# Optimization experiments

Hardware: AMD Instinct MI355X
Metric: run time of the kernel (lower is better)

Reference implementation:

```python
import jax, jax.numpy as jnp
import numpy as np

B, S, D, H = 4, 2048, 512, 8
HD = D // H
POOL_HEADS = 8


def setup_inputs() -> dict:
    key = jax.random.key(0)
    ks = iter(jax.random.split(key, 32))
    p = {}
    p['x'] = jax.random.normal(next(ks), (B, S, D), dtype=jnp.float32)
    p['mask'] = jnp.zeros((B, S), dtype=jnp.float32)  # key_padding_mask (1.0 = padded)
    s = 1.0 / np.sqrt(D)
    for layer in ('1', '2'):
        for name in ('q', 'k', 'v', 'o'):
            p[f'{name}{layer}_w'] = jax.random.normal(next(ks), (D, D), dtype=jnp.float32) * s
            p[f'{name}{layer}_b'] = jnp.zeros((D,), dtype=jnp.float32)
    p['ln1_g'] = jnp.ones((D,), jnp.float32); p['ln1_b'] = jnp.zeros((D,), jnp.float32)
    p['ffn_w1'] = jax.random.normal(next(ks), (D, D), dtype=jnp.float32) * s
    p['ffn_b1'] = jnp.zeros((D,), jnp.float32)
    p['ffn_w2'] = jax.random.normal(next(ks), (D, D), dtype=jnp.float32) * s
    p['ffn_b2'] = jnp.zeros((D,), jnp.float32)
    p['ln2_g'] = jnp.ones((D,), jnp.float32); p['ln2_b'] = jnp.zeros((D,), jnp.float32)
    p['pool_w'] = jax.random.normal(next(ks), (D, POOL_HEADS), dtype=jnp.float32) * s
    p['pool_b'] = jnp.zeros((POOL_HEADS,), jnp.float32)
    return p


def _layernorm(x, g, b, eps=1e-5):
    mu = jnp.mean(x, axis=-1, keepdims=True)
    var = jnp.var(x, axis=-1, keepdims=True)
    return (x - mu) * jax.lax.rsqrt(var + eps) * g + b


def _mha(x, mask, qw, qb, kw, kb, vw, vb, ow, ob):
    b, s, d = x.shape
    q = (x @ qw + qb).reshape(b, s, H, HD)
    k = (x @ kw + kb).reshape(b, s, H, HD)
    v = (x @ vw + vb).reshape(b, s, H, HD)
    scores = jnp.einsum('bihd,bjhd->bhij', q, k) / jnp.sqrt(jnp.float32(HD))
    scores = scores - mask[:, None, None, :] * 1e30  # key_padding_mask
    w = jax.nn.softmax(scores, axis=-1)  # dropout is identity at eval
    out = jnp.einsum('bhij,bjhd->bihd', w, v).reshape(b, s, d)
    return out @ ow + ob


def _pool(x, mask, pw, pb):
    alpha = jax.nn.leaky_relu(x @ pw + pb)            # [B,S,POOL_HEADS]
    alpha = alpha + mask[:, :, None] * -1e16
    alpha = jax.nn.softmax(alpha, axis=1)             # softmax over sequence
    # sum over heads of alpha_h * x, then sum over sequence
    return jnp.einsum('bs,bsd->bd', alpha.sum(axis=-1), x)


def reference(x, mask,
              q1_w, q1_b, k1_w, k1_b, v1_w, v1_b, o1_w, o1_b,
              q2_w, q2_b, k2_w, k2_b, v2_w, v2_b, o2_w, o2_b,
              ln1_g, ln1_b, ffn_w1, ffn_b1, ffn_w2, ffn_b2,
              ln2_g, ln2_b, pool_w, pool_b):
    # F.normalize(x, p=2, dim=-1)
    x = x / jnp.maximum(jnp.linalg.norm(x, axis=-1, keepdims=True), 1e-12)
    h = _mha(x, mask, q1_w, q1_b, k1_w, k1_b, v1_w, v1_b, o1_w, o1_b)
    h = _layernorm(h, ln1_g, ln1_b)
    h = jax.nn.relu(h @ ffn_w1 + ffn_b1) @ ffn_w2 + ffn_b2
    h = _mha(h, mask, q2_w, q2_b, k2_w, k2_b, v2_w, v2_b, o2_w, o2_b)
    h = _layernorm(h, ln2_g, ln2_b)
    return _pool(h, mask, pool_w, pool_b)  # [B, D] patch_feature (cls=False -> logit is None)
```

## Files before the change

kernel.cpp:

```cpp
#include <hip/hip_runtime.h>
#include <hip/hip_bf16.h>
#include <stdint.h>

#define DEVI __device__ __forceinline__

typedef float f32x4 __attribute__((ext_vector_type(4)));
typedef float f32x16 __attribute__((ext_vector_type(16)));
typedef short bf16x8 __attribute__((ext_vector_type(8)));

typedef __attribute__((address_space(3))) unsigned int as3_u32;
typedef __attribute__((address_space(1))) unsigned int as1_u32;

DEVI void gload16(const void* g, void* l) {
  __builtin_amdgcn_global_load_lds((const as1_u32*)g, (as3_u32*)l, 16, 0, 0);
}

DEVI unsigned short bf16r(float f) {
  union { float f; unsigned int u; } v; v.f = f;
  unsigned int u = v.u;
  return (unsigned short)((u + 0x7FFFu + ((u >> 16) & 1u)) >> 16);
}

DEVI unsigned int pkbf16(float a, float b) {
  __hip_bfloat162 h = __float22bfloat162_rn(make_float2(a, b));
  return *(unsigned int*)&h;
}

struct PrepArgs {
  const float* w[10];
  const float* b1[3];
  const float* b2[3];
};

__global__ __launch_bounds__(256) void prep_kernel(PrepArgs pa, unsigned short* wt,
                                                   float* qb1, float* qb2) {
  __shared__ float lt[64][65];
  const int slot = blockIdx.z;
  const int n0 = blockIdx.x * 64, k0 = blockIdx.y * 64;
  const float* W = pa.w[slot];
  for (int it = 0; it < 16; it++) {
    int idx = it * 256 + threadIdx.x;
    int kr = idx >> 6, nc = idx & 63;
    lt[kr][nc] = W[(long)(k0 + kr) * 512 + n0 + nc];
  }
  __syncthreads();
  unsigned short* dst = wt + (long)slot * 512 * 512;
  for (int it = 0; it < 16; it++) {
    int idx = it * 256 + threadIdx.x;
    int nr = idx >> 6, kc = idx & 63;
    dst[(long)(n0 + nr) * 512 + k0 + kc] = bf16r(lt[kc][nr]);
  }
  if (blockIdx.x == 0 && blockIdx.y == 0) {
    if (slot < 3) {
      for (int i = threadIdx.x; i < 512; i += 256) qb1[slot * 512 + i] = pa.b1[slot][i];
    } else if (slot >= 6 && slot < 9) {
      for (int i = threadIdx.x; i < 512; i += 256) qb2[(slot - 6) * 512 + i] = pa.b2[slot - 6][i];
    }
  }
}

__global__ __launch_bounds__(256) void l2norm_kernel(const float* __restrict__ x,
                                                     unsigned short* __restrict__ xn) {
  const long row = blockIdx.x;
  const float* xr = x + row * 512;
  float v0 = xr[threadIdx.x], v1 = xr[threadIdx.x + 256];
  float ss = v0 * v0 + v1 * v1;
  #pragma unroll
  for (int off = 32; off > 0; off >>= 1) ss += __shfl_down(ss, off, 64);
  __shared__ float red[4];
  __shared__ float sc[1];
  int w = threadIdx.x >> 6, ln = threadIdx.x & 63;
  if (ln == 0) red[w] = ss;
  __syncthreads();
  if (threadIdx.x == 0) {
    float S = red[0] + red[1] + red[2] + red[3];
    sc[0] = 1.0f / fmaxf(sqrtf(S), 1e-12f);
  }
  __syncthreads();
  float s = sc[0];
  xn[row * 512 + threadIdx.x] = bf16r(v0 * s);
  xn[row * 512 + threadIdx.x + 256] = bf16r(v1 * s);
}

template <int EPI>
__global__ __launch_bounds__(256) void gemm_bt(const unsigned short* __restrict__ A,
                                               const unsigned short* __restrict__ Bt,
                                               const float* __restrict__ bias,
                                               void* __restrict__ Cv, int K, int N,
                                               unsigned short* __restrict__ vtout) {
  __shared__ unsigned short ldsA[128 * 64];
  __shared__ unsigned short ldsB[128 * 64];
  const int tid = threadIdx.x, w = tid >> 6, ln = tid & 63;
  const int bm = blockIdx.x, bn = blockIdx.y;
  const int wm = (w >> 1) * 64, wn = (w & 1) * 64;
  const f32x4 zf = {0.f, 0.f, 0.f, 0.f};
  f32x4 acc[4][4];
  #pragma unroll
  for (int i = 0; i < 4; i++)
    #pragma unroll
    for (int j = 0; j < 4; j++) acc[i][j] = zf;
  const int r8 = ln >> 3, s8 = ln & 7;
  for (int kt = 0; kt < K; kt += 64) {
    #pragma unroll
    for (int i = 0; i < 4; i++) {
      int row = w * 32 + i * 8 + r8;
      gload16(A + (long)(bm * 128 + row) * K + kt + s8 * 8, &ldsA[(w * 32 + i * 8) * 64]);
      gload16(Bt + (long)(bn * 128 + row) * K + kt + s8 * 8, &ldsB[(w * 32 + i * 8) * 64]);
    }
    __syncthreads();
    #pragma unroll
    for (int kk = 0; kk < 2; kk++) {
      bf16x8 af[4], bfr[4];
      #pragma unroll
      for (int mf = 0; mf < 4; mf++) {
        int row = wm + mf * 16 + (ln & 15);
        af[mf] = *(const bf16x8*)&ldsA[row * 64 + kk * 32 + (ln >> 4) * 8];
      }
      #pragma unroll
      for (int nf = 0; nf < 4; nf++) {
        int row = wn + nf * 16 + (ln & 15);
        bfr[nf] = *(const bf16x8*)&ldsB[row * 64 + kk * 32 + (ln >> 4) * 8];
      }
      #pragma unroll
      for (int mf = 0; mf < 4; mf++)
        #pragma unroll
        for (int nf = 0; nf < 4; nf++)
          acc[mf][nf] = __builtin_amdgcn_mfma_f32_16x16x32_bf16(af[mf], bfr[nf], acc[mf][nf], 0, 0, 0);
    }
    __syncthreads();
  }
  const int g = ln >> 4, c = ln & 15;
  #pragma unroll
  for (int mf = 0; mf < 4; mf++) {
    #pragma unroll
    for (int nf = 0; nf < 4; nf++) {
      int col = bn * 128 + wn + nf * 16 + c;
      float bv = bias[col];
      if (EPI == 3 && col >= 1024) {
        long row0 = bm * 128 + wm + mf * 16 + g * 4;
        int b = (int)(row0 >> 11), s = (int)(row0 & 2047);
        int vc = col - 1024, h = vc >> 6, hd = vc & 63;
        ushort4 o;
        o.x = bf16r(acc[mf][nf][0] + bv);
        o.y = bf16r(acc[mf][nf][1] + bv);
        o.z = bf16r(acc[mf][nf][2] + bv);
        o.w = bf16r(acc[mf][nf][3] + bv);
        *(ushort4*)(vtout + ((long)((b * 8 + h) * 64 + hd)) * 2048 + s) = o;
      } else {
        #pragma unroll
        for (int j = 0; j < 4; j++) {
          long row = bm * 128 + wm + mf * 16 + g * 4 + j;
          float v = acc[mf][nf][j] + bv;
          if (EPI == 2) v = v > 0.f ? v : 0.f;
          if (EPI == 0)
            ((float*)Cv)[row * N + col] = v;
          else
            ((unsigned short*)Cv)[row * N + col] = bf16r(v);
        }
      }
    }
  }
}

template <int EPI>
__global__ __launch_bounds__(256) void gemm_bt64(const unsigned short* __restrict__ A,
                                                 const unsigned short* __restrict__ Bt,
                                                 const float* __restrict__ bias,
                                                 void* __restrict__ Cv, int K, int N) {
  __shared__ unsigned short ldsA[128 * 64];
  __shared__ unsigned short ldsB[64 * 64];
  const int tid = threadIdx.x, w = tid >> 6, ln = tid & 63;
  const int bm = blockIdx.x, bn = blockIdx.y;
  const int wm = (w >> 1) * 64, wn = (w & 1) * 32;
  const f32x4 zf = {0.f, 0.f, 0.f, 0.f};
  f32x4 acc[4][2];
  #pragma unroll
  for (int i = 0; i < 4; i++)
    #pragma unroll
    for (int j = 0; j < 2; j++) acc[i][j] = zf;
  const int r8 = ln >> 3, s8 = ln & 7;
  for (int kt = 0; kt < K; kt += 64) {
    #pragma unroll
    for (int i = 0; i < 6; i++) {
      int jj = w * 6 + i;
      if (jj < 16) {
        gload16(A + (long)(bm * 128 + jj * 8 + r8) * K + kt + s8 * 8, &ldsA[jj * 512]);
      } else {
        int jb = jj - 16;
        gload16(Bt + (long)(bn * 64 + jb * 8 + r8) * K + kt + s8 * 8, &ldsB[jb * 512]);
      }
    }
    __syncthreads();
    #pragma unroll
    for (int kk = 0; kk < 2; kk++) {
      bf16x8 af[4], bfr[2];
      #pragma unroll
      for (int mf = 0; mf < 4; mf++)
        af[mf] = *(const bf16x8*)&ldsA[(wm + mf * 16 + (ln & 15)) * 64 + kk * 32 + (ln >> 4) * 8];
      #pragma unroll
      for (int nf = 0; nf < 2; nf++)
        bfr[nf] = *(const bf16x8*)&ldsB[(wn + nf * 16 + (ln & 15)) * 64 + kk * 32 + (ln >> 4) * 8];
      #pragma unroll
      for (int mf = 0; mf < 4; mf++)
        #pragma unroll
        for (int nf = 0; nf < 2; nf++)
          acc[mf][nf] = __builtin_amdgcn_mfma_f32_16x16x32_bf16(af[mf], bfr[nf], acc[mf][nf], 0, 0, 0);
    }
    __syncthreads();
  }
  const int g = ln >> 4, c = ln & 15;
  #pragma unroll
  for (int mf = 0; mf < 4; mf++) {
    #pragma unroll
    for (int nf = 0; nf < 2; nf++) {
      int col = bn * 64 + wn + nf * 16 + c;
      float bv = bias[col];
      #pragma unroll
      for (int j = 0; j < 4; j++) {
        long row = bm * 128 + wm + mf * 16 + g * 4 + j;
        float v = acc[mf][nf][j] + bv;
        if (EPI == 2) v = v > 0.f ? v : 0.f;
        if (EPI == 0)
          ((float*)Cv)[row * N + col] = v;
        else
          ((unsigned short*)Cv)[row * N + col] = bf16r(v);
      }
    }
  }
}

__global__ __launch_bounds__(256, 4) void attn_kernel(
    const unsigned short* __restrict__ qkv,
    const unsigned short* __restrict__ vt,
    const float* __restrict__ mask,
    unsigned short* __restrict__ ao) {
  const int tid = threadIdx.x, w = tid >> 6, ln = tid & 63;
  const int lo = ln & 31, hi = ln >> 5;
  const int bid = blockIdx.x + 16 * blockIdx.y;
  const int swz = (bid & 7) * 64 + (bid >> 3);
  const int qb = swz & 15, bh = swz >> 4;
  const int b = bh >> 3, h = bh & 7;
  const int q0 = qb * 128 + w * 32;
  const unsigned short* qp = qkv + (long)(b * 2048) * 1536 + h * 64;
  const unsigned short* kp = qp + 512;
  const unsigned short* vtp = vt + (long)bh * 64 * 2048;
  const float* mp = mask + b * 2048;

  __shared__ unsigned short sbuf[2][4096];
  __shared__ float mbuf[2048];
  __shared__ int mflag;

  {
    float acc = 0.f;
    #pragma unroll
    for (int i = 0; i < 8; i++) {
      float mv = mp[i * 256 + tid];
      mbuf[i * 256 + tid] = mv;
      acc += fabsf(mv);
    }
    if (tid == 0) mflag = 0;
    __syncthreads();
    if (acc != 0.f) mflag = 1;
    __syncthreads();
  }
  const bool anymask = (mflag != 0);

  const int jj0 = w * 2;
  const char *src0, *src1;
  long step;
  if (w < 2) {
    int r0 = jj0 * 8 + (ln >> 3), r1 = r0 + 8, s = ln & 7;
    src0 = (const char*)kp + 2L * ((long)r0 * 1536 + ((s ^ (r0 & 7)) * 8));
    src1 = (const char*)kp + 2L * ((long)r1 * 1536 + ((s ^ (r1 & 7)) * 8));
    step = 32L * 1536 * 2;
  } else {
    int j0 = (w - 2) * 2;
    int r0 = j0 * 16 + (ln >> 2), r1 = r0 + 16, s = ln & 3;
    src0 = (const char*)vtp + 2L * ((long)r0 * 2048 + ((s ^ ((r0 >> 1) & 3)) * 8));
    src1 = (const char*)vtp + 2L * ((long)r1 * 2048 + ((s ^ ((r1 >> 1) & 3)) * 8));
    step = 64;
  }
  unsigned short* const d0a = &sbuf[0][jj0 * 512];
  unsigned short* const d0b = d0a + 512;
  unsigned short* const d1a = &sbuf[1][jj0 * 512];
  unsigned short* const d1b = d1a + 512;

  int koffe[4];
  #pragma unroll
  for (int t = 0; t < 4; t++)
    koffe[t] = lo * 64 + (((t * 2 + hi) ^ (lo & 7)) * 8);
  int voffe[4];
  #pragma unroll
  for (int stt = 0; stt < 2; stt++)
    #pragma unroll
    for (int tau = 0; tau < 2; tau++) {
      int vr = tau * 32 + lo;
      voffe[stt * 2 + tau] = 2048 + vr * 32 + ((((stt * 2 + hi) ^ ((vr >> 1) & 3))) * 8);
    }

  bf16x8 qf[4];
  #pragma unroll
  for (int t = 0; t < 4; t++)
    qf[t] = *(const bf16x8*)(qp + (long)(q0 + lo) * 1536 + t * 16 + hi * 8);

  f32x16 oacc[2];
  #pragma unroll
  for (int t = 0; t < 2; t++)
    #pragma unroll
    for (int r = 0; r < 16; r++) oacc[t][r] = 0.f;
  float lsum = 0.f;
  const f32x16 zf16 = oacc[0];
  const float SC = 0.18033688011112042f;

  gload16(src0, d0a);
  gload16(src1, d0b);
  src0 += step; src1 += step;

#define ATTN_BODY(CURB, DA, DB, ITOFF, STAGE_NEXT)                              \
  {                                                                             \
    if (STAGE_NEXT) {                                                           \
      gload16(src0, DA);                                                        \
      gload16(src1, DB);                                                        \
      src0 += step; src1 += step;                                               \
      asm volatile("s_waitcnt vmcnt(2)" ::: "memory");                          \
    } else {                                                                    \
      asm volatile("s_waitcnt vmcnt(0)" ::: "memory");                          \
    }                                                                           \
    __builtin_amdgcn_s_barrier();                                               \
    __builtin_amdgcn_sched_barrier(0);                                          \
    f32x16 sacc = zf16;                                                         \
    _Pragma("unroll")                                                           \
    for (int t = 0; t < 4; t++) {                                               \
      bf16x8 kf = *(const bf16x8*)&sbuf[CURB][koffe[t]];                        \
      sacc = __builtin_amdgcn_mfma_f32_32x32x16_bf16(kf, qf[t], sacc, 0, 0, 0); \
    }                                                                           \
    float e[16];                                                                \
    _Pragma("unroll")                                                           \
    for (int r = 0; r < 16; r++) e[r] = sacc[r] * SC;                           \
    if (anymask) {                                                              \
      float mval = mbuf[(ITOFF) + lo];                                          \
      _Pragma("unroll")                                                         \
      for (int r = 0; r < 16; r++)                                              \
        e[r] -= 1.4426950408889634e30f *                                        \
                __shfl(mval, (r & 3) + 8 * (r >> 2) + 4 * hi, 64);              \
    }                                                                           \
    _Pragma("unroll")                                                           \
    for (int r = 0; r < 16; r++) e[r] = __builtin_amdgcn_exp2f(e[r]);           \
    _Pragma("unroll")                                                           \
    for (int r = 0; r < 16; r++) lsum += e[r];                                  \
    unsigned int cv[8];                                                         \
    _Pragma("unroll")                                                           \
    for (int i = 0; i < 8; i++) cv[i] = pkbf16(e[2 * i], e[2 * i + 1]);         \
    _Pragma("unroll")                                                           \
    for (int stt = 0; stt < 2; stt++) {                                         \
      unsigned int pf[4];                                                       \
      {                                                                         \
        auto r0_ = __builtin_amdgcn_permlane32_swap(cv[stt * 4 + 0],            \
                                                    cv[stt * 4 + 2], false, false); \
        auto r1_ = __builtin_amdgcn_permlane32_swap(cv[stt * 4 + 1],            \
                                                    cv[stt * 4 + 3], false, false); \
        pf[0] = r0_[0]; pf[1] = r1_[0]; pf[2] = r0_[1]; pf[3] = r1_[1];         \
      }                                                                         \
      bf16x8 pfr = *(const bf16x8*)pf;                                          \
      _Pragma("unroll")                                                         \
      for (int tau = 0; tau < 2; tau++) {                                       \
        bf16x8 vf = *(const bf16x8*)&sbuf[CURB][voffe[stt * 2 + tau]];          \
        oacc[tau] = __builtin_amdgcn_mfma_f32_32x32x16_bf16(vf, pfr, oacc[tau], 0, 0, 0); \
      }                                                                         \
    }                                                                           \
    __builtin_amdgcn_sched_barrier(0);                                          \
    __builtin_amdgcn_s_barrier();                                               \
  }

  for (int it2 = 0; it2 < 32; it2++) {
    ATTN_BODY(0, d1a, d1b, it2 * 64, 1)
    ATTN_BODY(1, d0a, d0b, it2 * 64 + 32, (it2 < 31))
  }
#undef ATTN_BODY

  lsum += __shfl_xor(lsum, 32, 64);
  const float inv = 1.f / lsum;
  unsigned short* ob = ao + ((long)(b * 2048) + q0 + lo) * 512 + h * 64;
  #pragma unroll
  for (int tau = 0; tau < 2; tau++) {
    #pragma unroll
    for (int j = 0; j < 4; j++) {
      ushort4 o;
      o.x = bf16r(oacc[tau][4 * j + 0] * inv);
      o.y = bf16r(oacc[tau][4 * j + 1] * inv);
      o.z = bf16r(oacc[tau][4 * j + 2] * inv);
      o.w = bf16r(oacc[tau][4 * j + 3] * inv);
      *(ushort4*)(ob + tau * 32 + j * 8 + hi * 4) = o;
    }
  }
}

__global__ __launch_bounds__(256) void ln_kernel(const float* __restrict__ in,
                                                 const float* __restrict__ gam,
                                                 const float* __restrict__ bet,
                                                 unsigned short* __restrict__ out) {
  const long row = blockIdx.x;
  const float* x = in + row * 512;
  float v0 = x[threadIdx.x], v1 = x[threadIdx.x + 256];
  float s = v0 + v1, ss = v0 * v0 + v1 * v1;
  #pragma unroll
  for (int off = 32; off > 0; off >>= 1) {
    s += __shfl_down(s, off, 64);
    ss += __shfl_down(ss, off, 64);
  }
  __shared__ float red[8];
  __shared__ float mv[2];
  int w = threadIdx.x >> 6, ln = threadIdx.x & 63;
  if (ln == 0) { red[w] = s; red[w + 4] = ss; }
  __syncthreads();
  if (threadIdx.x == 0) {
    float S = red[0] + red[1] + red[2] + red[3];
    float SS = red[4] + red[5] + red[6] + red[7];
    float mu = S * (1.f / 512.f);
    float var = SS * (1.f / 512.f) - mu * mu;
    mv[0] = mu;
    mv[1] = rsqrtf(var + 1e-5f);
  }
  __syncthreads();
  float mu = mv[0], rs = mv[1];
  float o0 = (v0 - mu) * rs * gam[threadIdx.x] + bet[threadIdx.x];
  float o1 = (v1 - mu) * rs * gam[threadIdx.x + 256] + bet[threadIdx.x + 256];
  out[row * 512 + threadIdx.x] = bf16r(o0);
  out[row * 512 + threadIdx.x + 256] = bf16r(o1);
}

__global__ __launch_bounds__(256) void ln2_alpha_kernel(const float* __restrict__ in,
                                                        const float* __restrict__ gam,
                                                        const float* __restrict__ bet,
                                                        const float* __restrict__ pw,
                                                        const float* __restrict__ pbias,
                                                        const float* __restrict__ mask,
                                                        float* __restrict__ out,
                                                        float* __restrict__ alpha) {
  const long row = blockIdx.x;
  const float* x = in + row * 512;
  float v0 = x[threadIdx.x], v1 = x[threadIdx.x + 256];
  float s = v0 + v1, ss = v0 * v0 + v1 * v1;
  #pragma unroll
  for (int off = 32; off > 0; off >>= 1) {
    s += __shfl_down(s, off, 64);
    ss += __shfl_down(ss, off, 64);
  }
  __shared__ float red[8];
  __shared__ float mv[2];
  __shared__ float pr[4][8];
  int w = threadIdx.x >> 6, ln = threadIdx.x & 63;
  if (ln == 0) { red[w] = s; red[w + 4] = ss; }
  __syncthreads();
  if (threadIdx.x == 0) {
    float S = red[0] + red[1] + red[2] + red[3];
    float SS = red[4] + red[5] + red[6] + red[7];
    float mu = S * (1.f / 512.f);
    float var = SS * (1.f / 512.f) - mu * mu;
    mv[0] = mu;
    mv[1] = rsqrtf(var + 1e-5f);
  }
  __syncthreads();
  float mu = mv[0], rs = mv[1];
  float o0 = (v0 - mu) * rs * gam[threadIdx.x] + bet[threadIdx.x];
  float o1 = (v1 - mu) * rs * gam[threadIdx.x + 256] + bet[threadIdx.x + 256];
  out[row * 512 + threadIdx.x] = o0;
  out[row * 512 + threadIdx.x + 256] = o1;
  float p[8];
  const float* w0 = pw + threadIdx.x * 8;
  const float* w1 = pw + (threadIdx.x + 256) * 8;
  #pragma unroll
  for (int k = 0; k < 8; k++) p[k] = o0 * w0[k] + o1 * w1[k];
  #pragma unroll
  for (int off = 32; off > 0; off >>= 1)
    #pragma unroll
    for (int k = 0; k < 8; k++) p[k] += __shfl_down(p[k], off, 64);
  if (ln == 0)
    #pragma unroll
    for (int k = 0; k < 8; k++) pr[w][k] = p[k];
  __syncthreads();
  if (threadIdx.x < 8) {
    float a = pr[0][threadIdx.x] + pr[1][threadIdx.x] + pr[2][threadIdx.x] + pr[3][threadIdx.x]
              + pbias[threadIdx.x];
    a = a < 0.f ? 0.01f * a : a;
    alpha[row * 8 + threadIdx.x] = a + mask[row] * (-1e16f);
  }
}

__global__ __launch_bounds__(256) void stats_kernel(const float* __restrict__ alpha,
                                                    float* __restrict__ stats) {
  int b = blockIdx.x >> 3, ph = blockIdx.x & 7;
  const float* a = alpha + (long)b * 2048 * 8 + ph;
  __shared__ float rr[4];
  __shared__ float mm[1];
  int w = threadIdx.x >> 6, ln = threadIdx.x & 63;
  float m = -1e38f;
  for (int s = threadIdx.x; s < 2048; s += 256) m = fmaxf(m, a[(long)s * 8]);
  #pragma unroll
  for (int off = 32; off > 0; off >>= 1) m = fmaxf(m, __shfl_down(m, off, 64));
  if (ln == 0) rr[w] = m;
  __syncthreads();
  if (threadIdx.x == 0) mm[0] = fmaxf(fmaxf(rr[0], rr[1]), fmaxf(rr[2], rr[3]));
  __syncthreads();
  float M = mm[0];
  float sum = 0.f;
  for (int s = threadIdx.x; s < 2048; s += 256) sum += __expf(a[(long)s * 8] - M);
  #pragma unroll
  for (int off = 32; off > 0; off >>= 1) sum += __shfl_down(sum, off, 64);
  __syncthreads();
  if (ln == 0) rr[w] = sum;
  __syncthreads();
  if (threadIdx.x == 0) {
    stats[blockIdx.x * 2] = M;
    stats[blockIdx.x * 2 + 1] = rr[0] + rr[1] + rr[2] + rr[3];
  }
}

__global__ __launch_bounds__(256) void pool_kernel(const float* __restrict__ h,
                                                   const float* __restrict__ alpha,
                                                   const float* __restrict__ stats,
                                                   float* __restrict__ partial) {
  int b = blockIdx.x >> 3, sc = blockIdx.x & 7;
  int s0 = sc * 256;
  __shared__ float wb[256];
  {
    long s = s0 + threadIdx.x;
    const float* a = alpha + ((long)b * 2048 + s) * 8;
    float wsum = 0.f;
    #pragma unroll
    for (int ph = 0; ph < 8; ph++) {
      float M = stats[(b * 8 + ph) * 2], Sm = stats[(b * 8 + ph) * 2 + 1];
      wsum += __expf(a[ph] - M) / Sm;
    }
    wb[threadIdx.x] = wsum;
  }
  __syncthreads();
  float a0 = 0.f, a1 = 0.f;
  const float* hb = h + ((long)b * 2048 + s0) * 512;
  for (int i = 0; i < 256; i++) {
    float wv = wb[i];
    a0 += wv * hb[(long)i * 512 + threadIdx.x];
    a1 += wv * hb[(long)i * 512 + threadIdx.x + 256];
  }
  partial[(long)blockIdx.x * 512 + threadIdx.x] = a0;
  partial[(long)blockIdx.x * 512 + threadIdx.x + 256] = a1;
}

__global__ __launch_bounds__(256) void pool_final(const float* __restrict__ partial,
                                                  float* __restrict__ out) {
  int b = blockIdx.x;
  float a0 = 0.f, a1 = 0.f;
  #pragma unroll
  for (int sc = 0; sc < 8; sc++) {
    a0 += partial[(long)(b * 8 + sc) * 512 + threadIdx.x];
    a1 += partial[(long)(b * 8 + sc) * 512 + threadIdx.x + 256];
  }
  out[b * 512 + threadIdx.x] = a0;
  out[b * 512 + threadIdx.x + 256] = a1;
}

extern "C" void kernel_launch(void* const* d_in, const int* in_sizes, int n_in,
                              void* d_out, int out_size, void* d_ws, size_t ws_size,
                              hipStream_t stream) {
  (void)in_sizes; (void)n_in; (void)out_size;
  if (ws_size < 92274688UL) return;

  const float* x    = (const float*)d_in[0];
  const float* mask = (const float*)d_in[1];
  const float* q1w = (const float*)d_in[2];  const float* q1b = (const float*)d_in[3];
  const float* k1w = (const float*)d_in[4];  const float* k1b = (const float*)d_in[5];
  const float* v1w = (const float*)d_in[6];  const float* v1b = (const float*)d_in[7];
  const float* o1w = (const float*)d_in[8];  const float* o1b = (const float*)d_in[9];
  const float* q2w = (const float*)d_in[10]; const float* q2b = (const float*)d_in[11];
  const float* k2w = (const float*)d_in[12]; const float* k2b = (const float*)d_in[13];
  const float* v2w = (const float*)d_in[14]; const float* v2b = (const float*)d_in[15];
  const float* o2w = (const float*)d_in[16]; const float* o2b = (const float*)d_in[17];
  const float* ln1g = (const float*)d_in[18]; const float* ln1b = (const float*)d_in[19];
  const float* fw1 = (const float*)d_in[20]; const float* fb1 = (const float*)d_in[21];
  const float* fw2 = (const float*)d_in[22]; const float* fb2 = (const float*)d_in[23];
  const float* ln2g = (const float*)d_in[24]; const float* ln2b = (const float*)d_in[25];
  const float* poolw = (const float*)d_in[26]; const float* poolb = (const float*)d_in[27];

  char* ws = (char*)d_ws;
  unsigned short* Wt  = (unsigned short*)(ws + 0);
  float* qb1          = (float*)(ws + 5242880);
  float* qb2          = (float*)(ws + 5249024);
  float* stats        = (float*)(ws + 5255168);
  float* alpha        = (float*)(ws + 5255424);
  float* partial      = (float*)(ws + 5517568);
  unsigned short* qkv = (unsigned short*)(ws + 8388608);
  unsigned short* vt  = (unsigned short*)(ws + 33554432);
  unsigned short* ao  = (unsigned short*)(ws + 41943040);
  float* t            = (float*)(ws + 50331648);
  unsigned short* xn  = (unsigned short*)(ws + 67108864);
  unsigned short* h1  = (unsigned short*)(ws + 75497472);
  unsigned short* f   = (unsigned short*)(ws + 83886080);
  unsigned short* h2  = xn;

  PrepArgs pa;
  pa.w[0] = q1w; pa.w[1] = k1w; pa.w[2] = v1w; pa.w[3] = o1w; pa.w[4] = fw1;
  pa.w[5] = fw2; pa.w[6] = q2w; pa.w[7] = k2w; pa.w[8] = v2w; pa.w[9] = o2w;
  pa.b1[0] = q1b; pa.b1[1] = k1b; pa.b1[2] = v1b;
  pa.b2[0] = q2b; pa.b2[1] = k2b; pa.b2[2] = v2b;

  prep_kernel<<<dim3(8, 8, 10), 256, 0, stream>>>(pa, Wt, qb1, qb2);
  l2norm_kernel<<<8192, 256, 0, stream>>>(x, xn);

  gemm_bt<3><<<dim3(64, 12), 256, 0, stream>>>(xn, Wt, qb1, qkv, 512, 1536, vt);
  attn_kernel<<<dim3(16, 32), 256, 0, stream>>>(qkv, vt, mask, ao);
  gemm_bt64<0><<<dim3(64, 8), 256, 0, stream>>>(ao, Wt + 3L * 512 * 512, o1b, t, 512, 512);
  ln_kernel<<<8192, 256, 0, stream>>>(t, ln1g, ln1b, h1);
  gemm_bt64<2><<<dim3(64, 8), 256, 0, stream>>>(h1, Wt + 4L * 512 * 512, fb1, f, 512, 512);
  gemm_bt64<1><<<dim3(64, 8), 256, 0, stream>>>(f, Wt + 5L * 512 * 512, fb2, h2, 512, 512);

  gemm_bt<3><<<dim3(64, 12), 256, 0, stream>>>(h2, Wt + 6L * 512 * 512, qb2, qkv, 512, 1536, vt);
  attn_kernel<<<dim3(16, 32), 256, 0, stream>>>(qkv, vt, mask, ao);
  gemm_bt64<0><<<dim3(64, 8), 256, 0, stream>>>(ao, Wt + 9L * 512 * 512, o2b, t, 512, 512);
  ln2_alpha_kernel<<<8192, 256, 0, stream>>>(t, ln2g, ln2b, poolw, poolb, mask, t, alpha);

  stats_kernel<<<32, 256, 0, stream>>>(alpha, stats);
  pool_kernel<<<32, 256, 0, stream>>>(t, alpha, stats, partial);
  pool_final<<<4, 256, 0, stream>>>(partial, (float*)d_out);
}
```

Measured before the change: 292.5 us.

## Fuse prep with l2norm, store intermediates in bf16, fold softmax stats into pool, raise MFMA priority

Merges the weight-prep and L2-norm launches into one grid, and removes the separate stats kernel by recomputing per-head max and sum inside each pool block. The out-projection and LN2 outputs are now stored as bf16 instead of fp32, which halves the traffic for the intermediate activations. Attention wraps its MFMA loops in s_setprio to favour matrix issue. The changes trade some precision and redundant stats work in the pool blocks for fewer launches and fewer bytes moved.

```diff
diff --git a/kernel.cpp b/kernel.cpp
--- a/kernel.cpp
+++ b/kernel.cpp
@@ -19,6 +19,12 @@
   union { float f; unsigned int u; } v; v.f = f;
   unsigned int u = v.u;
   return (unsigned short)((u + 0x7FFFu + ((u >> 16) & 1u)) >> 16);
+}
+
+DEVI float bf2f(unsigned short u) {
+  unsigned int x = ((unsigned int)u) << 16;
+  union { unsigned int u; float f; } v; v.u = x;
+  return v.f;
 }
 
 DEVI unsigned int pkbf16(float a, float b) {
@@ -32,54 +38,56 @@
   const float* b2[3];
 };
 
-__global__ __launch_bounds__(256) void prep_kernel(PrepArgs pa, unsigned short* wt,
-                                                   float* qb1, float* qb2) {
-  __shared__ float lt[64][65];
-  const int slot = blockIdx.z;
-  const int n0 = blockIdx.x * 64, k0 = blockIdx.y * 64;
-  const float* W = pa.w[slot];
-  for (int it = 0; it < 16; it++) {
-    int idx = it * 256 + threadIdx.x;
-    int kr = idx >> 6, nc = idx & 63;
-    lt[kr][nc] = W[(long)(k0 + kr) * 512 + n0 + nc];
-  }
-  __syncthreads();
-  unsigned short* dst = wt + (long)slot * 512 * 512;
-  for (int it = 0; it < 16; it++) {
-    int idx = it * 256 + threadIdx.x;
-    int nr = idx >> 6, kc = idx & 63;
-    dst[(long)(n0 + nr) * 512 + k0 + kc] = bf16r(lt[kc][nr]);
-  }
-  if (blockIdx.x == 0 && blockIdx.y == 0) {
-    if (slot < 3) {
-      for (int i = threadIdx.x; i < 512; i += 256) qb1[slot * 512 + i] = pa.b1[slot][i];
-    } else if (slot >= 6 && slot < 9) {
-      for (int i = threadIdx.x; i < 512; i += 256) qb2[(slot - 6) * 512 + i] = pa.b2[slot - 6][i];
-    }
-  }
-}
-
-__global__ __launch_bounds__(256) void l2norm_kernel(const float* __restrict__ x,
-                                                     unsigned short* __restrict__ xn) {
-  const long row = blockIdx.x;
-  const float* xr = x + row * 512;
-  float v0 = xr[threadIdx.x], v1 = xr[threadIdx.x + 256];
-  float ss = v0 * v0 + v1 * v1;
-  #pragma unroll
-  for (int off = 32; off > 0; off >>= 1) ss += __shfl_down(ss, off, 64);
-  __shared__ float red[4];
-  __shared__ float sc[1];
-  int w = threadIdx.x >> 6, ln = threadIdx.x & 63;
-  if (ln == 0) red[w] = ss;
-  __syncthreads();
-  if (threadIdx.x == 0) {
-    float S = red[0] + red[1] + red[2] + red[3];
-    sc[0] = 1.0f / fmaxf(sqrtf(S), 1e-12f);
-  }
-  __syncthreads();
-  float s = sc[0];
-  xn[row * 512 + threadIdx.x] = bf16r(v0 * s);
-  xn[row * 512 + threadIdx.x + 256] = bf16r(v1 * s);
+__global__ __launch_bounds__(256) void prep_l2norm_kernel(PrepArgs pa, unsigned short* wt,
+                                                          float* qb1, float* qb2,
+                                                          const float* __restrict__ x,
+                                                          unsigned short* __restrict__ xn) {
+  const int bid = blockIdx.x;
+  if (bid < 640) {
+    __shared__ float lt[64][65];
+    const int slot = bid >> 6, r = bid & 63;
+    const int n0 = (r & 7) * 64, k0 = (r >> 3) * 64;
+    const float* W = pa.w[slot];
+    for (int it = 0; it < 16; it++) {
+      int idx = it * 256 + threadIdx.x;
+      int kr = idx >> 6, nc = idx & 63;
+      lt[kr][nc] = W[(long)(k0 + kr) * 512 + n0 + nc];
+    }
+    __syncthreads();
+    unsigned short* dst = wt + (long)slot * 512 * 512;
+    for (int it = 0; it < 16; it++) {
+      int idx = it * 256 + threadIdx.x;
+      int nr = idx >> 6, kc = idx & 63;
+      dst[(long)(n0 + nr) * 512 + k0 + kc] = bf16r(lt[kc][nr]);
+    }
+    if (r == 0) {
+      if (slot < 3) {
+        for (int i = threadIdx.x; i < 512; i += 256) qb1[slot * 512 + i] = pa.b1[slot][i];
+      } else if (slot >= 6 && slot < 9) {
+        for (int i = threadIdx.x; i < 512; i += 256) qb2[(slot - 6) * 512 + i] = pa.b2[slot - 6][i];
+      }
+    }
+  } else {
+    const long row = bid - 640;
+    const float* xr = x + row * 512;
+    float v0 = xr[threadIdx.x], v1 = xr[threadIdx.x + 256];
+    float ss = v0 * v0 + v1 * v1;
+    #pragma unroll
+    for (int off = 32; off > 0; off >>= 1) ss += __shfl_down(ss, off, 64);
+    __shared__ float red[4];
+    __shared__ float sc[1];
+    int w = threadIdx.x >> 6, ln = threadIdx.x & 63;
+    if (ln == 0) red[w] = ss;
+    __syncthreads();
+    if (threadIdx.x == 0) {
+      float S = red[0] + red[1] + red[2] + red[3];
+      sc[0] = 1.0f / fmaxf(sqrtf(S), 1e-12f);
+    }
+    __syncthreads();
+    float s = sc[0];
+    xn[row * 512 + threadIdx.x] = bf16r(v0 * s);
+    xn[row * 512 + threadIdx.x + 256] = bf16r(v1 * s);
+  }
 }
 
 template <int EPI>
@@ -152,10 +160,7 @@
           long row = bm * 128 + wm + mf * 16 + g * 4 + j;
           float v = acc[mf][nf][j] + bv;
           if (EPI == 2) v = v > 0.f ? v : 0.f;
-          if (EPI == 0)
-            ((float*)Cv)[row * N + col] = v;
-          else
-            ((unsigned short*)Cv)[row * N + col] = bf16r(v);
+          ((unsigned short*)Cv)[row * N + col] = bf16r(v);
         }
       }
     }
@@ -220,10 +225,7 @@
         long row = bm * 128 + wm + mf * 16 + g * 4 + j;
         float v = acc[mf][nf][j] + bv;
         if (EPI == 2) v = v > 0.f ? v : 0.f;
-        if (EPI == 0)
-          ((float*)Cv)[row * N + col] = v;
-        else
-          ((unsigned short*)Cv)[row * N + col] = bf16r(v);
+        ((unsigned short*)Cv)[row * N + col] = bf16r(v);
       }
     }
   }
@@ -329,11 +331,13 @@
     __builtin_amdgcn_s_barrier();                                               \
     __builtin_amdgcn_sched_barrier(0);                                          \
     f32x16 sacc = zf16;                                                         \
+    __builtin_amdgcn_s_setprio(1);                                              \
     _Pragma("unroll")                                                           \
     for (int t = 0; t < 4; t++) {                                               \
       bf16x8 kf = *(const bf16x8*)&sbuf[CURB][koffe[t]];                        \
       sacc = __builtin_amdgcn_mfma_f32_32x32x16_bf16(kf, qf[t], sacc, 0, 0, 0); \
     }                                                                           \
+    __builtin_amdgcn_s_setprio(0);                                              \
     float e[16];                                                                \
     _Pragma("unroll")                                                           \
     for (int r = 0; r < 16; r++) e[r] = sacc[r] * SC;                           \
@@ -362,11 +366,13 @@
         pf[0] = r0_[0]; pf[1] = r1_[0]; pf[2] = r0_[1]; pf[3] = r1_[1];         \
       }                                                                         \
       bf16x8 pfr = *(const bf16x8*)pf;                                          \
+      __builtin_amdgcn_s_setprio(1);                                            \
       _Pragma("unroll")                                                         \
       for (int tau = 0; tau < 2; tau++) {                                       \
         bf16x8 vf = *(const bf16x8*)&sbuf[CURB][voffe[stt * 2 + tau]];          \
         oacc[tau] = __builtin_amdgcn_mfma_f32_32x32x16_bf16(vf, pfr, oacc[tau], 0, 0, 0); \
       }                                                                         \
+      __builtin_amdgcn_s_setprio(0);                                            \
     }                                                                           \
     __builtin_amdgcn_sched_barrier(0);                                          \
     __builtin_amdgcn_s_barrier();                                               \
@@ -395,13 +401,13 @@
   }
 }
 
-__global__ __launch_bounds__(256) void ln_kernel(const float* __restrict__ in,
+__global__ __launch_bounds__(256) void ln_kernel(const unsigned short* __restrict__ in,
                                                  const float* __restrict__ gam,
                                                  const float* __restrict__ bet,
                                                  unsigned short* __restrict__ out) {
   const long row = blockIdx.x;
-  const float* x = in + row * 512;
-  float v0 = x[threadIdx.x], v1 = x[threadIdx.x + 256];
+  const unsigned short* x = in + row * 512;
+  float v0 = bf2f(x[threadIdx.x]), v1 = bf2f(x[threadIdx.x + 256]);
   float s = v0 + v1, ss = v0 * v0 + v1 * v1;
   #pragma unroll
   for (int off = 32; off > 0; off >>= 1) {
@@ -429,17 +435,17 @@
   out[row * 512 + threadIdx.x + 256] = bf16r(o1);
 }
 
-__global__ __launch_bounds__(256) void ln2_alpha_kernel(const float* __restrict__ in,
+__global__ __launch_bounds__(256) void ln2_alpha_kernel(const unsigned short* __restrict__ in,
                                                         const float* __restrict__ gam,
                                                         const float* __restrict__ bet,
                                                         const float* __restrict__ pw,
                                                         const float* __restrict__ pbias,
                                                         const float* __restrict__ mask,
-                                                        float* __restrict__ out,
+                                                        unsigned short* __restrict__ out,
                                                         float* __restrict__ alpha) {
   const long row = blockIdx.x;
-  const float* x = in + row * 512;
-  float v0 = x[threadIdx.x], v1 = x[threadIdx.x + 256];
+  const unsigned short* x = in + row * 512;
+  float v0 = bf2f(x[threadIdx.x]), v1 = bf2f(x[threadIdx.x + 256]);
   float s = v0 + v1, ss = v0 * v0 + v1 * v1;
   #pragma unroll
   for (int off = 32; off > 0; off >>= 1) {
@@ -464,8 +470,8 @@
   float mu = mv[0], rs = mv[1];
   float o0 = (v0 - mu) * rs * gam[threadIdx.x] + bet[threadIdx.x];
   float o1 = (v1 - mu) * rs * gam[threadIdx.x + 256] + bet[threadIdx.x + 256];
-  out[row * 512 + threadIdx.x] = o0;
-  out[row * 512 + threadIdx.x + 256] = o1;
+  out[row * 512 + threadIdx.x] = bf16r(o0);
+  out[row * 512 + threadIdx.x + 256] = bf16r(o1);
   float p[8];
   const float* w0 = pw + threadIdx.x * 8;
   const float* w1 = pw + (threadIdx.x + 256) * 8;
@@ -487,60 +493,71 @@
   }
 }
 
-__global__ __launch_bounds__(256) void stats_kernel(const float* __restrict__ alpha,
-                                                    float* __restrict__ stats) {
-  int b = blockIdx.x >> 3, ph = blockIdx.x & 7;
-  const float* a = alpha + (long)b * 2048 * 8 + ph;
-  __shared__ float rr[4];
-  __shared__ float mm[1];
-  int w = threadIdx.x >> 6, ln = threadIdx.x & 63;
-  float m = -1e38f;
-  for (int s = threadIdx.x; s < 2048; s += 256) m = fmaxf(m, a[(long)s * 8]);
-  #pragma unroll
-  for (int off = 32; off > 0; off >>= 1) m = fmaxf(m, __shfl_down(m, off, 64));
-  if (ln == 0) rr[w] = m;
-  __syncthreads();
-  if (threadIdx.x == 0) mm[0] = fmaxf(fmaxf(rr[0], rr[1]), fmaxf(rr[2], rr[3]));
-  __syncthreads();
-  float M = mm[0];
-  float sum = 0.f;
-  for (int s = threadIdx.x; s < 2048; s += 256) sum += __expf(a[(long)s * 8] - M);
-  #pragma unroll
-  for (int off = 32; off > 0; off >>= 1) sum += __shfl_down(sum, off, 64);
-  __syncthreads();
-  if (ln == 0) rr[w] = sum;
-  __syncthreads();
-  if (threadIdx.x == 0) {
-    stats[blockIdx.x * 2] = M;
-    stats[blockIdx.x * 2 + 1] = rr[0] + rr[1] + rr[2] + rr[3];
-  }
-}
-
-__global__ __launch_bounds__(256) void pool_kernel(const float* __restrict__ h,
+__global__ __launch_bounds__(256) void pool_kernel(const unsigned short* __restrict__ h,
                                                    const float* __restrict__ alpha,
-                                                   const float* __restrict__ stats,
                                                    float* __restrict__ partial) {
   int b = blockIdx.x >> 3, sc = blockIdx.x & 7;
+  int w = threadIdx.x >> 6, ln = threadIdx.x & 63;
+  __shared__ float red[4][8];
+  __shared__ float Ms[8], Ss[8];
+  __shared__ float wb[256];
+  const float* ab = alpha + (long)b * 2048 * 8;
+  float m[8];
+  #pragma unroll
+  for (int k = 0; k < 8; k++) m[k] = -1e38f;
+  for (int s = threadIdx.x; s < 2048; s += 256) {
+    const float* a = ab + (long)s * 8;
+    #pragma unroll
+    for (int k = 0; k < 8; k++) m[k] = fmaxf(m[k], a[k]);
+  }
+  #pragma unroll
+  for (int off = 32; off > 0; off >>= 1)
+    #pragma unroll
+    for (int k = 0; k < 8; k++) m[k] = fmaxf(m[k], __shfl_down(m[k], off, 64));
+  if (ln == 0)
+    #pragma unroll
+    for (int k = 0; k < 8; k++) red[w][k] = m[k];
+  __syncthreads();
+  if (threadIdx.x < 8)
+    Ms[threadIdx.x] = fmaxf(fmaxf(red[0][threadIdx.x], red[1][threadIdx.x]),
+                            fmaxf(red[2][threadIdx.x], red[3][threadIdx.x]));
+  __syncthreads();
+  float sm[8];
+  #pragma unroll
+  for (int k = 0; k < 8; k++) sm[k] = 0.f;
+  for (int s = threadIdx.x; s < 2048; s += 256) {
+    const float* a = ab + (long)s * 8;
+    #pragma unroll
+    for (int k = 0; k < 8; k++) sm[k] += __expf(a[k] - Ms[k]);
+  }
+  #pragma unroll
+  for (int off = 32; off > 0; off >>= 1)
+    #pragma unroll
+    for (int k = 0; k < 8; k++) sm[k] += __shfl_down(sm[k], off, 64);
+  __syncthreads();
+  if (ln == 0)
+    #pragma unroll
+    for (int k = 0; k < 8; k++) red[w][k] = sm[k];
+  __syncthreads();
+  if (threadIdx.x < 8)
+    Ss[threadIdx.x] = red[0][threadIdx.x] + red[1][threadIdx.x] +
+                      red[2][threadIdx.x] + red[3][threadIdx.x];
+  __syncthreads();
   int s0 = sc * 256;
-  __shared__ float wb[256];
   {
-    long s = s0 + threadIdx.x;
-    const float* a = alpha + ((long)b * 2048 + s) * 8;
+    const float* a = ab + (long)(s0 + threadIdx.x) * 8;
     float wsum = 0.f;
     #pragma unroll
-    for (int ph = 0; ph < 8; ph++) {
-      float M = stats[(b * 8 + ph) * 2], Sm = stats[(b * 8 + ph) * 2 + 1];
-      wsum += __expf(a[ph] - M) / Sm;
-    }
+    for (int ph = 0; ph < 8; ph++) wsum += __expf(a[ph] - Ms[ph]) / Ss[ph];
     wb[threadIdx.x] = wsum;
   }
   __syncthreads();
   float a0 = 0.f, a1 = 0.f;
-  const float* hb = h + ((long)b * 2048 + s0) * 512;
+  const unsigned short* hb = h + ((long)b * 2048 + s0) * 512;
   for (int i = 0; i < 256; i++) {
     float wv = wb[i];
-    a0 += wv * hb[(long)i * 512 + threadIdx.x];
-    a1 += wv * hb[(long)i * 512 + threadIdx.x + 256];
+    a0 += wv * bf2f(hb[(long)i * 512 + threadIdx.x]);
+    a1 += wv * bf2f(hb[(long)i * 512 + threadIdx.x + 256]);
   }
   partial[(long)blockIdx.x * 512 + threadIdx.x] = a0;
   partial[(long)blockIdx.x * 512 + threadIdx.x + 256] = a1;
@@ -585,13 +602,12 @@
   unsigned short* Wt  = (unsigned short*)(ws + 0);
   float* qb1          = (float*)(ws + 5242880);
   float* qb2          = (float*)(ws + 5249024);
-  float* stats        = (float*)(ws + 5255168);
   float* alpha        = (float*)(ws + 5255424);
   float* partial      = (float*)(ws + 5517568);
   unsigned short* qkv = (unsigned short*)(ws + 8388608);
   unsigned short* vt  = (unsigned short*)(ws + 33554432);
   unsigned short* ao  = (unsigned short*)(ws + 41943040);
-  float* t            = (float*)(ws + 50331648);
+  unsigned short* tb  = (unsigned short*)(ws + 50331648);
   unsigned short* xn  = (unsigned short*)(ws + 67108864);
   unsigned short* h1  = (unsigned short*)(ws + 75497472);
   unsigned short* f   = (unsigned short*)(ws + 83886080);
@@ -603,22 +619,20 @@
   pa.b1[0] = q1b; pa.b1[1] = k1b; pa.b1[2] = v1b;
   pa.b2[0] = q2b; pa.b2[1] = k2b; pa.b2[2] = v2b;
 
-  prep_kernel<<<dim3(8, 8, 10), 256, 0, stream>>>(pa, Wt, qb1, qb2);
-  l2norm_kernel<<<8192, 256, 0, stream>>>(x, xn);
+  prep_l2norm_kernel<<<8832, 256, 0, stream>>>(pa, Wt, qb1, qb2, x, xn);
 
   gemm_bt<3><<<dim3(64, 12), 256, 0, stream>>>(xn, Wt, qb1, qkv, 512, 1536, vt);
   attn_kernel<<<dim3(16, 32), 256, 0, stream>>>(qkv, vt, mask, ao);
-  gemm_bt64<0><<<dim3(64, 8), 256, 0, stream>>>(ao, Wt + 3L * 512 * 512, o1b, t, 512, 512);
-  ln_kernel<<<8192, 256, 0, stream>>>(t, ln1g, ln1b, h1);
+  gemm_bt64<1><<<dim3(64, 8), 256, 0, stream>>>(ao, Wt + 3L * 512 * 512, o1b, tb, 512, 512);
+  ln_kernel<<<8192, 256, 0, stream>>>(tb, ln1g, ln1b, h1);
   gemm_bt64<2><<<dim3(64, 8), 256, 0, stream>>>(h1, Wt + 4L * 512 * 512, fb1, f, 512, 512);
   gemm_bt64<1><<<dim3(64, 8), 256, 0, stream>>>(f, Wt + 5L * 512 * 512, fb2, h2, 512, 512);
 
   gemm_bt<3><<<dim3(64, 12), 256, 0, stream>>>(h2, Wt + 6L * 512 * 512, qb2, qkv, 512, 1536, vt);
   attn_kernel<<<dim3(16, 32), 256, 0, stream>>>(qkv, vt, mask, ao);
-  gemm_bt64<0><<<dim3(64, 8), 256, 0, stream>>>(ao, Wt + 9L * 512 * 512, o2b, t, 512, 512);
-  ln2_alpha_kernel<<<8192, 256, 0, stream>>>(t, ln2g, ln2b, poolw, poolb, mask, t, alpha);
-
-  stats_kernel<<<32, 256, 0, stream>>>(alpha, stats);
-  pool_kernel<<<32, 256, 0, stream>>>(t, alpha, stats, partial);
+  gemm_bt64<1><<<dim3(64, 8), 256, 0, stream>>>(ao, Wt + 9L * 512 * 512, o2b, tb, 512, 512);
+  ln2_alpha_kernel<<<8192, 256, 0, stream>>>(tb, ln2g, ln2b, poolw, poolb, mask, tb, alpha);
+
+  pool_kernel<<<32, 256, 0, stream>>>(tb, alpha, partial);
   pool_final<<<4, 256, 0, stream>>>(partial, (float*)d_out);
 }
```

After: 293.7 us. No clear change (+0.4%).
